# Optimization experiments

Hardware: AMD Instinct MI355X
Metric: run time of the kernel (lower is better)

## Reference

```python
import jax, jax.numpy as jnp
import numpy as np

B, N, D, R, K = 16384, 20, 64, 3, 64  # batch, triples per sample, embed dim, n_relations, r_dim


def setup_inputs() -> dict:
    key = jax.random.key(0)
    ks = jax.random.split(key, 8)
    # xavier_normal std for [2D, K] matrices: sqrt(2/(2D+K))
    std_w = float(np.sqrt(2.0 / (2 * D + K)))
    std_r = float(np.sqrt(2.0 / (R + K)))
    return {
        "u_emb": jax.random.normal(ks[0], (B, D), dtype=jnp.float32),
        "i_emb": jax.random.normal(ks[1], (B, D), dtype=jnp.float32),
        "a_emb": jax.random.normal(ks[2], (B, N, D), dtype=jnp.float32),
        "o_emb": jax.random.normal(ks[3], (B, N, D), dtype=jnp.float32),
        "s": jax.random.randint(ks[4], (B, N), 0, R, dtype=jnp.int64),
        "w_uir": jax.random.normal(ks[5], (R, 2 * D, K), dtype=jnp.float32) * std_w,
        "w_aor": jax.random.normal(ks[6], (R, 2 * D, K), dtype=jnp.float32) * std_w,
        "r_vec": jax.random.normal(ks[7], (R, K), dtype=jnp.float32) * std_r,
    }


def reference(u_emb, i_emb, a_emb, o_emb, s, w_uir, w_aor, r_vec):
    # transr predictor, bpr loss
    ui_in = jnp.concatenate([u_emb, i_emb], axis=-1)          # [B, 2D]
    ao_in = jnp.concatenate([a_emb, o_emb], axis=-1)          # [B, N, 2D]
    n_rel = w_uir.shape[0]
    ui_emb = jnp.zeros(ao_in.shape[:2] + (w_uir.shape[-1],), dtype=ui_in.dtype)  # [B, N, K]
    ao_emb = jnp.zeros_like(ui_emb)
    for r_idx in range(n_rel):  # small fixed relation count
        m = (s == r_idx)[..., None]                            # [B, N, 1]
        ui_r = ui_in @ w_uir[r_idx] + r_vec[r_idx]             # [B, K]
        ao_r = jnp.einsum("bnd,dk->bnk", ao_in, w_aor[r_idx])  # [B, N, K]
        ui_emb = jnp.where(m, ui_r[:, None, :], ui_emb)
        ao_emb = jnp.where(m, ao_r, ao_emb)
    pred = jnp.sum(ui_emb * ao_emb, axis=-1)                   # [B, N]
    return pred
```

## Files before the change

### kernel.cpp

```cpp
#include <hip/hip_runtime.h>
#include <hip/hip_bf16.h>

#define BB   16384
#define NN   20
#define NREL 3

typedef __attribute__((ext_vector_type(8))) short  short8;
typedef __attribute__((ext_vector_type(4))) float  f32x4;

__device__ __forceinline__ float lo16(unsigned int u) {
    union { unsigned int x; float f; } c; c.x = u << 16; return c.f;
}
__device__ __forceinline__ float hi16(unsigned int u) {
    union { unsigned int x; float f; } c; c.x = u & 0xFFFF0000u; return c.f;
}

__device__ __forceinline__ unsigned short f2bu(float f) {
    union { float f; unsigned int u; } x;
    x.f = f;
    unsigned int r = x.u + 0x7FFFu + ((x.u >> 16) & 1u);
    return (unsigned short)(r >> 16);
}

__global__ __launch_bounds__(256) void k_precompute(
    const float* __restrict__ w_uir,
    const float* __restrict__ w_aor,
    const float* __restrict__ r_vec,
    unsigned short* __restrict__ McatT,
    float* __restrict__ cvec)
{
    int idx = blockIdx.x * 256 + threadIdx.x;
    if (idx < NREL * 128 * 128) {
        int d = idx & 127;
        int e = (idx >> 7) & 127;
        int r = idx >> 14;
        const float4* pu = reinterpret_cast<const float4*>(w_uir + (r * 128 + d) * 64);
        const float4* pa = reinterpret_cast<const float4*>(w_aor + (r * 128 + e) * 64);
        float acc = 0.f;
        #pragma unroll
        for (int k = 0; k < 16; ++k) {
            float4 a = pu[k], b = pa[k];
            acc += a.x * b.x + a.y * b.y + a.z * b.z + a.w * b.w;
        }
        McatT[(r * 128 + e) * 128 + d] = f2bu(acc);
    } else if (idx < NREL * 128 * 128 + NREL * 128) {
        int j = idx - NREL * 128 * 128;
        int r = j >> 7, e = j & 127;
        const float4* pr = reinterpret_cast<const float4*>(r_vec + r * 64);
        const float4* pa = reinterpret_cast<const float4*>(w_aor + (r * 128 + e) * 64);
        float acc = 0.f;
        #pragma unroll
        for (int k = 0; k < 16; ++k) {
            float4 a = pr[k], b = pa[k];
            acc += a.x * b.x + a.y * b.y + a.z * b.z + a.w * b.w;
        }
        cvec[j] = acc;
    }
}

#define K3_BLOCKS (BB / 16)
#define UI_OFF 0
#define VP_OFF 4096
#define AO_OFF 16384
#define K3_LDS 57344

__device__ __forceinline__ void stage_ao(
    const float* __restrict__ a_emb, const float* __restrict__ o_emb,
    char* lds, size_t t0s, int wv, int lane)
{
    const char* asrc = (const char*)a_emb + t0s * 256;
    const char* osrc = (const char*)o_emb + t0s * 256;
    #pragma unroll
    for (int i = 0; i < 5; ++i) {
        int seg = i * 4 + wv;
        __builtin_amdgcn_global_load_lds(
            (const unsigned int*)(asrc + seg * 1024 + (size_t)lane * 16),
            (unsigned int*)(lds + AO_OFF + seg * 1024), 16, 0, 0);
    }
    #pragma unroll
    for (int i = 0; i < 5; ++i) {
        int seg = i * 4 + wv;
        __builtin_amdgcn_global_load_lds(
            (const unsigned int*)(osrc + seg * 1024 + (size_t)lane * 16),
            (unsigned int*)(lds + AO_OFF + 20480 + seg * 1024), 16, 0, 0);
    }
}

__device__ __forceinline__ void consume_slice(
    const char* lds, int sl, size_t t0s,
    const int* sv, int g, int sub, float* __restrict__ out)
{
    #pragma unroll
    for (int p = 0; p < 5; ++p) {
        const int ltrip = p * 16 + g;
        const int bl    = ltrip / NN;
        const int brow  = sl * 4 + bl;
        const int svv   = sv[p];
        float4 af = *(const float4*)(lds + AO_OFF + ltrip * 256 + sub * 16);
        float4 of = *(const float4*)(lds + AO_OFF + 20480 + ltrip * 256 + sub * 16);
        uint2  wa = *(const uint2*)(lds + VP_OFF + brow * 768 + svv * 256 + sub * 8);
        uint2  wo = *(const uint2*)(lds + VP_OFF + brow * 768 + svv * 256 + 128 + sub * 8);
        float r = af.x * lo16(wa.x) + af.y * hi16(wa.x)
                + af.z * lo16(wa.y) + af.w * hi16(wa.y)
                + of.x * lo16(wo.x) + of.y * hi16(wo.x)
                + of.z * lo16(wo.y) + of.w * hi16(wo.y);
        r += __shfl_xor(r, 1, 64);
        r += __shfl_xor(r, 2, 64);
        r += __shfl_xor(r, 4, 64);
        r += __shfl_xor(r, 8, 64);
        if (sub == 0) out[t0s + ltrip] = r;
    }
}

__global__ __launch_bounds__(256) void k_fused(
    const float* __restrict__ u_emb,
    const float* __restrict__ i_emb,
    const float* __restrict__ a_emb,
    const float* __restrict__ o_emb,
    const int* __restrict__ s,
    const unsigned short* __restrict__ McatT,
    const float* __restrict__ cvec,
    float* __restrict__ out)
{
    __shared__ __align__(16) char lds[K3_LDS];

    const int tid  = threadIdx.x;
    const int bid  = blockIdx.x;
    const int wv   = tid >> 6;
    const int lane = tid & 63;
    const int g    = tid >> 4;
    const int sub  = tid & 15;
    const int lr   = lane & 15;
    const int lk   = (lane >> 4) * 8;

    const int    b0     = bid * 16;
    const size_t t0blk  = (size_t)bid * 320;

    stage_ao(a_emb, o_emb, lds, t0blk, wv, lane);
    int sv0[5];
    #pragma unroll
    for (int p = 0; p < 5; ++p) sv0[p] = s[t0blk + p * 16 + g];

    {
        const int r  = tid >> 4;
        const int c8 = (tid & 15) * 8;
        const float* src = (c8 < 64)
            ? (u_emb + (size_t)(b0 + r) * 64 + c8)
            : (i_emb + (size_t)(b0 + r) * 64 + (c8 - 64));
        float4 v0 = *(const float4*)(src);
        float4 v1 = *(const float4*)(src + 4);
        unsigned short h[8];
        h[0] = f2bu(v0.x); h[1] = f2bu(v0.y); h[2] = f2bu(v0.z); h[3] = f2bu(v0.w);
        h[4] = f2bu(v1.x); h[5] = f2bu(v1.y); h[6] = f2bu(v1.z); h[7] = f2bu(v1.w);
        *(ushort4*)(lds + UI_OFF + (r * 128 + c8) * 2)       = *(ushort4*)&h[0];
        *(ushort4*)(lds + UI_OFF + (r * 128 + c8) * 2 + 8)   = *(ushort4*)&h[4];
    }
    __syncthreads();

    const unsigned short* ui16 = (const unsigned short*)(lds + UI_OFF);
    #pragma unroll
    for (int nt = 0; nt < 6; ++nt) {
        const int col = wv * 96 + nt * 16 + lr;
        f32x4 acc = {0.f, 0.f, 0.f, 0.f};
        #pragma unroll
        for (int kk = 0; kk < 4; ++kk) {
            short8 afrag = *(const short8*)&ui16[lr * 128 + kk * 32 + lk];
            short8 bfrag = *(const short8*)(McatT + col * 128 + kk * 32 + lk);
            acc = __builtin_amdgcn_mfma_f32_16x16x32_bf16(afrag, bfrag, acc, 0, 0, 0);
        }
        const float cb = cvec[col];
        #pragma unroll
        for (int reg = 0; reg < 4; ++reg) {
            const int brow = (lane >> 4) * 4 + reg;
            *(unsigned short*)(lds + VP_OFF + brow * 768 + col * 2)
                = f2bu(acc[reg] + cb);
        }
    }
    __syncthreads();

    consume_slice(lds, 0, t0blk, sv0, g, sub, out);

    #pragma unroll
    for (int sl = 1; sl < 4; ++sl) {
        __syncthreads();
        const size_t t0s = t0blk + (size_t)sl * 80;
        stage_ao(a_emb, o_emb, lds, t0s, wv, lane);
        int sv[5];
        #pragma unroll
        for (int p = 0; p < 5; ++p) sv[p] = s[t0s + p * 16 + g];
        __syncthreads();
        consume_slice(lds, sl, t0s, sv, g, sub, out);
    }
}

extern "C" void kernel_launch(void* const* d_in, const int* in_sizes, int n_in,
                              void* d_out, int out_size, void* d_ws, size_t ws_size,
                              hipStream_t stream) {
    const float* u_emb = (const float*)d_in[0];
    const float* i_emb = (const float*)d_in[1];
    const float* a_emb = (const float*)d_in[2];
    const float* o_emb = (const float*)d_in[3];
    const int*   s     = (const int*)d_in[4];
    const float* w_uir = (const float*)d_in[5];
    const float* w_aor = (const float*)d_in[6];
    const float* r_vec = (const float*)d_in[7];
    float* out = (float*)d_out;

    char* ws = (char*)d_ws;
    unsigned short* McatT = (unsigned short*)ws;
    float*          cvec  = (float*)(ws + 98304);

    k_precompute<<<194, 256, 0, stream>>>(w_uir, w_aor, r_vec, McatT, cvec);
    k_fused<<<K3_BLOCKS, 256, 0, stream>>>(u_emb, i_emb, a_emb, o_emb, s,
                                           McatT, cvec, out);
}
```

Measured before the change: 46.40 us.

## Double-buffer a/o slices with prefetch and widen fused kernel to 512 threads

Splits the per-block triple stream into eight 40-triple slices held in two LDS buffers. The global-to-LDS load for the next slice is issued before the current slice is consumed, so loads overlap with compute instead of waiting behind a barrier. The block grows to 512 threads (8 waves), and the MFMA projection and u/i staging work are redistributed across the extra waves. Risks: the barrier at the end of each slice may still force a wait on all outstanding loads, which would limit the overlap. The extra threads also raise per-block resource use, which may lower occupancy.

```diff
diff --git a/kernel.cpp b/kernel.cpp
--- a/kernel.cpp
+++ b/kernel.cpp
@@ -61,45 +61,41 @@
 #define K3_BLOCKS (BB / 16)
 #define UI_OFF 0
 #define VP_OFF 4096
-#define AO_OFF 16384
+#define SL_OFF 16384
+#define SL_SZ  20480
 #define K3_LDS 57344
 
-__device__ __forceinline__ void stage_ao(
+__device__ __forceinline__ void dma_seg(
+    char* buf, const char* asrc, const char* osrc, int seg, int lane)
+{
+    const char* src = (seg < 10) ? (asrc + seg * 1024 + (size_t)lane * 16)
+                                 : (osrc + (seg - 10) * 1024 + (size_t)lane * 16);
+    __builtin_amdgcn_global_load_lds((const unsigned int*)src,
+                                     (unsigned int*)(buf + seg * 1024), 16, 0, 0);
+}
+
+__device__ __forceinline__ void stage_slice(
     const float* __restrict__ a_emb, const float* __restrict__ o_emb,
-    char* lds, size_t t0s, int wv, int lane)
+    char* buf, size_t t0s, int wv, int lane)
 {
     const char* asrc = (const char*)a_emb + t0s * 256;
     const char* osrc = (const char*)o_emb + t0s * 256;
-    #pragma unroll
-    for (int i = 0; i < 5; ++i) {
-        int seg = i * 4 + wv;
-        __builtin_amdgcn_global_load_lds(
-            (const unsigned int*)(asrc + seg * 1024 + (size_t)lane * 16),
-            (unsigned int*)(lds + AO_OFF + seg * 1024), 16, 0, 0);
-    }
-    #pragma unroll
-    for (int i = 0; i < 5; ++i) {
-        int seg = i * 4 + wv;
-        __builtin_amdgcn_global_load_lds(
-            (const unsigned int*)(osrc + seg * 1024 + (size_t)lane * 16),
-            (unsigned int*)(lds + AO_OFF + 20480 + seg * 1024), 16, 0, 0);
-    }
+    dma_seg(buf, asrc, osrc, wv, lane);
+    dma_seg(buf, asrc, osrc, wv + 8, lane);
+    if (wv < 4) dma_seg(buf, asrc, osrc, wv + 16, lane);
 }
 
 __device__ __forceinline__ void consume_slice(
-    const char* lds, int sl, size_t t0s,
-    const int* sv, int g, int sub, float* __restrict__ out)
-{
-    #pragma unroll
-    for (int p = 0; p < 5; ++p) {
-        const int ltrip = p * 16 + g;
-        const int bl    = ltrip / NN;
-        const int brow  = sl * 4 + bl;
-        const int svv   = sv[p];
-        float4 af = *(const float4*)(lds + AO_OFF + ltrip * 256 + sub * 16);
-        float4 of = *(const float4*)(lds + AO_OFF + 20480 + ltrip * 256 + sub * 16);
-        uint2  wa = *(const uint2*)(lds + VP_OFF + brow * 768 + svv * 256 + sub * 8);
-        uint2  wo = *(const uint2*)(lds + VP_OFF + brow * 768 + svv * 256 + 128 + sub * 8);
+    const char* lds, const char* buf, int sl, size_t t0s,
+    int sv0, int sv1, int g, int sub, float* __restrict__ out)
+{
+    {
+        const int ltrip = g;
+        const int brow  = sl * 2 + (ltrip / NN);
+        float4 af = *(const float4*)(buf + ltrip * 256 + sub * 16);
+        float4 of = *(const float4*)(buf + 10240 + ltrip * 256 + sub * 16);
+        uint2  wa = *(const uint2*)(lds + VP_OFF + brow * 768 + sv0 * 256 + sub * 8);
+        uint2  wo = *(const uint2*)(lds + VP_OFF + brow * 768 + sv0 * 256 + 128 + sub * 8);
         float r = af.x * lo16(wa.x) + af.y * hi16(wa.x)
                 + af.z * lo16(wa.y) + af.w * hi16(wa.y)
                 + of.x * lo16(wo.x) + of.y * hi16(wo.x)
@@ -110,9 +106,26 @@
         r += __shfl_xor(r, 8, 64);
         if (sub == 0) out[t0s + ltrip] = r;
     }
-}
-
-__global__ __launch_bounds__(256) void k_fused(
+    if (g < 8) {
+        const int ltrip = 32 + g;
+        const int brow  = sl * 2 + 1;
+        float4 af = *(const float4*)(buf + ltrip * 256 + sub * 16);
+        float4 of = *(const float4*)(buf + 10240 + ltrip * 256 + sub * 16);
+        uint2  wa = *(const uint2*)(lds + VP_OFF + brow * 768 + sv1 * 256 + sub * 8);
+        uint2  wo = *(const uint2*)(lds + VP_OFF + brow * 768 + sv1 * 256 + 128 + sub * 8);
+        float r = af.x * lo16(wa.x) + af.y * hi16(wa.x)
+                + af.z * lo16(wa.y) + af.w * hi16(wa.y)
+                + of.x * lo16(wo.x) + of.y * hi16(wo.x)
+                + of.z * lo16(wo.y) + of.w * hi16(wo.y);
+        r += __shfl_xor(r, 1, 64);
+        r += __shfl_xor(r, 2, 64);
+        r += __shfl_xor(r, 4, 64);
+        r += __shfl_xor(r, 8, 64);
+        if (sub == 0) out[t0s + ltrip] = r;
+    }
+}
+
+__global__ __launch_bounds__(512) void k_fused(
     const float* __restrict__ u_emb,
     const float* __restrict__ i_emb,
     const float* __restrict__ a_emb,
@@ -133,34 +146,30 @@
     const int lr   = lane & 15;
     const int lk   = (lane >> 4) * 8;
 
-    const int    b0     = bid * 16;
-    const size_t t0blk  = (size_t)bid * 320;
-
-    stage_ao(a_emb, o_emb, lds, t0blk, wv, lane);
-    int sv0[5];
-    #pragma unroll
-    for (int p = 0; p < 5; ++p) sv0[p] = s[t0blk + p * 16 + g];
+    const int    b0    = bid * 16;
+    const size_t t0blk = (size_t)bid * 320;
+
+    stage_slice(a_emb, o_emb, lds + SL_OFF, t0blk, wv, lane);
+    int svc0 = s[t0blk + g];
+    int svc1 = (g < 8) ? s[t0blk + 32 + g] : 0;
 
     {
-        const int r  = tid >> 4;
-        const int c8 = (tid & 15) * 8;
-        const float* src = (c8 < 64)
-            ? (u_emb + (size_t)(b0 + r) * 64 + c8)
-            : (i_emb + (size_t)(b0 + r) * 64 + (c8 - 64));
-        float4 v0 = *(const float4*)(src);
-        float4 v1 = *(const float4*)(src + 4);
-        unsigned short h[8];
-        h[0] = f2bu(v0.x); h[1] = f2bu(v0.y); h[2] = f2bu(v0.z); h[3] = f2bu(v0.w);
-        h[4] = f2bu(v1.x); h[5] = f2bu(v1.y); h[6] = f2bu(v1.z); h[7] = f2bu(v1.w);
-        *(ushort4*)(lds + UI_OFF + (r * 128 + c8) * 2)       = *(ushort4*)&h[0];
-        *(ushort4*)(lds + UI_OFF + (r * 128 + c8) * 2 + 8)   = *(ushort4*)&h[4];
+        const int r  = tid >> 5;
+        const int c4 = (tid & 31) * 4;
+        const float* src = (c4 < 64)
+            ? (u_emb + (size_t)(b0 + r) * 64 + c4)
+            : (i_emb + (size_t)(b0 + r) * 64 + (c4 - 64));
+        float4 v = *(const float4*)(src);
+        unsigned short h[4];
+        h[0] = f2bu(v.x); h[1] = f2bu(v.y); h[2] = f2bu(v.z); h[3] = f2bu(v.w);
+        *(ushort4*)(lds + UI_OFF + (r * 128 + c4) * 2) = *(ushort4*)&h[0];
     }
     __syncthreads();
 
     const unsigned short* ui16 = (const unsigned short*)(lds + UI_OFF);
     #pragma unroll
-    for (int nt = 0; nt < 6; ++nt) {
-        const int col = wv * 96 + nt * 16 + lr;
+    for (int nt = 0; nt < 3; ++nt) {
+        const int col = wv * 48 + nt * 16 + lr;
         f32x4 acc = {0.f, 0.f, 0.f, 0.f};
         #pragma unroll
         for (int kk = 0; kk < 4; ++kk) {
@@ -178,18 +187,20 @@
     }
     __syncthreads();
 
-    consume_slice(lds, 0, t0blk, sv0, g, sub, out);
-
     #pragma unroll
-    for (int sl = 1; sl < 4; ++sl) {
+    for (int sl = 0; sl < 8; ++sl) {
+        int svn0 = 0, svn1 = 0;
+        if (sl < 7) {
+            const size_t t0n = t0blk + (size_t)(sl + 1) * 40;
+            stage_slice(a_emb, o_emb, lds + SL_OFF + ((sl + 1) & 1) * SL_SZ,
+                        t0n, wv, lane);
+            svn0 = s[t0n + g];
+            svn1 = (g < 8) ? s[t0n + 32 + g] : 0;
+        }
+        consume_slice(lds, lds + SL_OFF + (sl & 1) * SL_SZ, sl,
+                      t0blk + (size_t)sl * 40, svc0, svc1, g, sub, out);
         __syncthreads();
-        const size_t t0s = t0blk + (size_t)sl * 80;
-        stage_ao(a_emb, o_emb, lds, t0s, wv, lane);
-        int sv[5];
-        #pragma unroll
-        for (int p = 0; p < 5; ++p) sv[p] = s[t0s + p * 16 + g];
-        __syncthreads();
-        consume_slice(lds, sl, t0s, sv, g, sub, out);
+        svc0 = svn0; svc1 = svn1;
     }
 }
 
@@ -211,6 +222,6 @@
     float*          cvec  = (float*)(ws + 98304);
 
     k_precompute<<<194, 256, 0, stream>>>(w_uir, w_aor, r_vec, McatT, cvec);
-    k_fused<<<K3_BLOCKS, 256, 0, stream>>>(u_emb, i_emb, a_emb, o_emb, s,
+    k_fused<<<K3_BLOCKS, 512, 0, stream>>>(u_emb, i_emb, a_emb, o_emb, s,
                                            McatT, cvec, out);
 }
```

After: 45.42 us. 2.1% less time.
